# Performance work log

Hardware: AMD Instinct MI355X
Metric: run time of the kernel (lower is better)

The kernel has to match this reference:

```python
import jax, jax.numpy as jnp
import numpy as np

N_NODES = 100000
N_EDGES = 1200000
NUM_GRAPHS = 128
IN_DIM = 5
HIDDEN = 64


def setup_inputs() -> dict:
    key = jax.random.key(0)
    ks = jax.random.split(key, 12)
    x = jax.random.normal(ks[0], (N_NODES, IN_DIM), dtype=jnp.float32)
    edge_index = jax.random.randint(ks[1], (2, N_EDGES), 0, N_NODES, dtype=jnp.int64 if jax.config.read('jax_enable_x64') else jnp.int32)
    batch = jnp.sort(jax.random.randint(ks[2], (N_NODES,), 0, NUM_GRAPHS, dtype=jnp.int32))
    s = lambda fan_in: 1.0 / np.sqrt(fan_in)
    return {
        'x': x,
        'edge_index': edge_index,
        'batch': batch,
        'w_rel1': jax.random.normal(ks[3], (IN_DIM, HIDDEN), dtype=jnp.float32) * s(IN_DIM),
        'b_rel1': jnp.zeros((HIDDEN,), dtype=jnp.float32),
        'w_root1': jax.random.normal(ks[4], (IN_DIM, HIDDEN), dtype=jnp.float32) * s(IN_DIM),
        'w_rel2': jax.random.normal(ks[5], (HIDDEN, HIDDEN), dtype=jnp.float32) * s(HIDDEN),
        'b_rel2': jnp.zeros((HIDDEN,), dtype=jnp.float32),
        'w_root2': jax.random.normal(ks[6], (HIDDEN, HIDDEN), dtype=jnp.float32) * s(HIDDEN),
        'w_h1': jax.random.normal(ks[7], (2 * HIDDEN, HIDDEN), dtype=jnp.float32) * s(2 * HIDDEN),
        'b_h1': jnp.zeros((HIDDEN,), dtype=jnp.float32),
        'w_h2': jax.random.normal(ks[8], (HIDDEN, 1), dtype=jnp.float32) * s(HIDDEN),
        'b_h2': jnp.zeros((1,), dtype=jnp.float32),
    }


def _graph_conv(x, src, dst, w_rel, b_rel, w_root):
    # PyG GraphConv (aggr='add'): out = aggr(x_src -> dst) @ W_rel + b_rel + x @ W_root
    agg = jax.ops.segment_sum(x[src], dst, num_segments=N_NODES)
    return agg @ w_rel + b_rel + x @ w_root


def reference(x, edge_index, batch,
              w_rel1, b_rel1, w_root1,
              w_rel2, b_rel2, w_root2,
              w_h1, b_h1, w_h2, b_h2):
    src, dst = edge_index[0], edge_index[1]
    h = jax.nn.relu(_graph_conv(x, src, dst, w_rel1, b_rel1, w_root1))
    h = jax.nn.relu(_graph_conv(h, src, dst, w_rel2, b_rel2, w_root2))
    # global add + mean pooling over graphs
    add_pool = jax.ops.segment_sum(h, batch, num_segments=NUM_GRAPHS)
    counts = jax.ops.segment_sum(jnp.ones((N_NODES,), h.dtype), batch, num_segments=NUM_GRAPHS)
    mean_pool = add_pool / jnp.maximum(counts, 1.0)[:, None]
    g = jnp.concatenate([mean_pool, add_pool], axis=1)  # [G, 2*HIDDEN]
    out = jax.nn.relu(g @ w_h1 + b_h1) @ w_h2 + b_h2
    return out.squeeze(-1)
```

## Files before the change

kernel.cpp:

```cpp
#include <hip/hip_runtime.h>
#include <hip/hip_bf16.h>

#define N_NODES    100000
#define N_EDGES    1200000
#define NUM_GRAPHS 128
#define IN_DIM     5
#define HIDDEN     64
#define M_TILES    (N_NODES / 16)
#define NI4        (N_EDGES / 4)

#define CB    782
#define CBLK  256
#define EPB   ((NI4 + CBLK - 1) / CBLK)
#define STCAP 3072

typedef __attribute__((ext_vector_type(8))) short short8;
typedef __attribute__((ext_vector_type(4))) float f32x4;
typedef __attribute__((ext_vector_type(2))) float f32x2;

#if defined(__has_builtin)
#if __has_builtin(__builtin_amdgcn_cvt_pk_f32_fp8)
#define HAS_HWF8 1
#endif
#endif

__device__ __forceinline__ unsigned short f2bs(float f) {
    union { float f; unsigned u; } v; v.f = f;
    return (unsigned short)((v.u + 0x7FFFu + ((v.u >> 16) & 1u)) >> 16);
}
__device__ __forceinline__ float bs2f(unsigned short s) {
    union { unsigned u; float f; } v; v.u = ((unsigned)s) << 16;
    return v.f;
}
__device__ __forceinline__ float blo(unsigned p) { return bs2f((unsigned short)(p & 0xffff)); }
__device__ __forceinline__ float bhi(unsigned p) { return bs2f((unsigned short)(p >> 16)); }
__device__ __forceinline__ unsigned pack2(float a, float b) {
    return ((unsigned)f2bs(b) << 16) | (unsigned)f2bs(a);
}

__device__ __forceinline__ unsigned char f2f8(float f) {
    union { float f; unsigned u; } v; v.f = f * 0x1p-120f;
    unsigned u = v.u + 0x7FFFFu + ((v.u >> 20) & 1u);
    return (unsigned char)(u >> 20);
}
__device__ __forceinline__ float f82f(unsigned b) {
    union { unsigned u; float f; } v; v.u = (b & 0x7Fu) << 20;
    return v.f * 0x1p120f;
}

__device__ __forceinline__ void acc8(float4& a, unsigned r) {
#ifdef HAS_HWF8
    f32x2 lo = __builtin_amdgcn_cvt_pk_f32_fp8((int)r, false);
    f32x2 hi = __builtin_amdgcn_cvt_pk_f32_fp8((int)r, true);
    a.x += lo[0]; a.y += lo[1]; a.z += hi[0]; a.w += hi[1];
#else
    a.x += f82f(r); a.y += f82f(r >> 8); a.z += f82f(r >> 16); a.w += f82f(r >> 24);
#endif
}


__global__ void coarse_count(const int* __restrict__ dst, int* __restrict__ gcnt,
                             const float* __restrict__ x, uint4* __restrict__ xb,
                             float* __restrict__ add_pool, int* __restrict__ ptr) {
    __shared__ int h[CB];
    int t = threadIdx.x, b = blockIdx.x;
    for (int i = t; i < CB; i += 256) h[i] = 0;
    __syncthreads();
    int i0 = b * EPB, i1 = min(i0 + EPB, NI4);
    for (int i = i0 + t; i < i1; i += 256) {
        int4 d = ((const int4*)dst)[i];
        atomicAdd(&h[d.x >> 7], 1);
        atomicAdd(&h[d.y >> 7], 1);
        atomicAdd(&h[d.z >> 7], 1);
        atomicAdd(&h[d.w >> 7], 1);
    }
    __syncthreads();
    for (int i = t; i < CB; i += 256) gcnt[b * CB + i] = h[i];

    for (int n = b * 256 + t; n < N_NODES; n += CBLK * 256) {
        const float* xr = x + (size_t)n * IN_DIM;
        uint4 o;
        o.x = pack2(xr[0], xr[1]);
        o.y = pack2(xr[2], xr[3]);
        o.z = pack2(xr[4], 0.0f);
        o.w = 0u;
        xb[n] = o;
    }
    if (b == 0) {
        for (int i = t; i < NUM_GRAPHS * HIDDEN; i += 256) add_pool[i] = 0.0f;
        if (t == 0) ptr[N_NODES] = N_EDGES;
    }
}

__global__ void block_scan(int* __restrict__ gcnt, int* __restrict__ btot) {
    __shared__ int s[CBLK];
    int k = blockIdx.x, t = threadIdx.x;
    int v = gcnt[t * CB + k];
    s[t] = v;
    __syncthreads();
    for (int off = 1; off < CBLK; off <<= 1) {
        int u = (t >= off) ? s[t - off] : 0;
        __syncthreads();
        s[t] += u;
        __syncthreads();
    }
    gcnt[t * CB + k] = s[t] - v;
    if (t == CBLK - 1) btot[k] = s[t];
}

__global__ void bucket_scan(const int* __restrict__ btot, int* __restrict__ bstart) {
    __shared__ int s[1024];
    int t = threadIdx.x;
    int v = (t < CB) ? btot[t] : 0;
    s[t] = v;
    __syncthreads();
    for (int off = 1; off < 1024; off <<= 1) {
        int u = (t >= off) ? s[t - off] : 0;
        __syncthreads();
        s[t] += u;
        __syncthreads();
    }
    if (t < CB) bstart[t] = s[t] - v;
    if (t == 0) bstart[CB] = N_EDGES;
}

__global__ void partition_k(const int* __restrict__ src, const int* __restrict__ dst,
                            const int* __restrict__ gcnt, const int* __restrict__ bstart,
                            int* __restrict__ part) {
    __shared__ int base[CB];
    __shared__ int h[CB];
    int t = threadIdx.x, b = blockIdx.x;
    for (int i = t; i < CB; i += 256) {
        base[i] = bstart[i] + gcnt[b * CB + i];
        h[i] = 0;
    }
    __syncthreads();
    int i0 = b * EPB, i1 = min(i0 + EPB, NI4);
    for (int i = i0 + t; i < i1; i += 256) {
        int4 s4 = ((const int4*)src)[i];
        int4 d4 = ((const int4*)dst)[i];
        int k, r;
        k = d4.x >> 7; r = atomicAdd(&h[k], 1); part[base[k] + r] = s4.x | ((d4.x & 127) << 17);
        k = d4.y >> 7; r = atomicAdd(&h[k], 1); part[base[k] + r] = s4.y | ((d4.y & 127) << 17);
        k = d4.z >> 7; r = atomicAdd(&h[k], 1); part[base[k] + r] = s4.z | ((d4.z & 127) << 17);
        k = d4.w >> 7; r = atomicAdd(&h[k], 1); part[base[k] + r] = s4.w | ((d4.w & 127) << 17);
    }
}

__global__ void fine_gather1(const int* __restrict__ part, const int* __restrict__ bstart,
                             int* __restrict__ ptr, int* __restrict__ esrc,
                             const uint4* __restrict__ xb,
                             const float* __restrict__ x,
                             const float* __restrict__ w_rel1,
                             const float* __restrict__ b_rel1,
                             const float* __restrict__ w_root1,
                             unsigned short* __restrict__ h1,
                             unsigned char* __restrict__ h1f8) {
    __shared__ int fh[128];
    __shared__ int fo[128];
    __shared__ int fr[128];
    __shared__ uint4 stage[STCAP];
    int k = blockIdx.x, t = threadIdx.x;
    int e0 = bstart[k], e1 = bstart[k + 1];
    int ne = e1 - e0;
    bool useLds = (ne <= STCAP);
    if (t < 128) { fh[t] = 0; fr[t] = 0; }
    __syncthreads();
    for (int e = e0 + t; e < e1; e += 256)
        atomicAdd(&fh[(part[e] >> 17) & 127], 1);
    __syncthreads();
    int v = (t < 128) ? fh[t] : 0;
    if (t < 128) fo[t] = v;
    __syncthreads();
    for (int off = 1; off < 128; off <<= 1) {
        int u = (t >= off && t < 128) ? fo[t - off] : 0;
        __syncthreads();
        if (t < 128) fo[t] += u;
        __syncthreads();
    }
    if (t < 128) {
        int excl = fo[t] - v;
        int n_t = (k << 7) + t;
        if (n_t < N_NODES) ptr[n_t] = e0 + excl;
        fh[t] = excl;
    }
    __syncthreads();
    for (int e = e0 + t; e < e1; e += 256) {
        int p = part[e];
        int d = (p >> 17) & 127;
        int s = p & 0x1FFFF;
        int r = atomicAdd(&fr[d], 1);
        int slot = fh[d] + r;
        esrc[e0 + slot] = s;
        if (useLds) stage[slot] = xb[s];
    }
    __syncthreads();

    int ql = t & 15;
    int g  = t >> 4;
    float wr[IN_DIM][4], wo[IN_DIM][4], bias[4];
#pragma unroll
    for (int j = 0; j < 4; ++j) {
        int ch = ql * 4 + j;
        bias[j] = b_rel1[ch];
#pragma unroll
        for (int kk = 0; kk < IN_DIM; ++kk) {
            wr[kk][j] = w_rel1[kk * HIDDEN + ch];
            wo[kk][j] = w_root1[kk * HIDDEN + ch];
        }
    }

    for (int nl = g; nl < 128; nl += 16) {
        int n = (k << 7) + nl;
        if (n >= N_NODES) break;
        int s0 = fh[nl];
        int s1 = (nl < 127) ? fh[nl + 1] : ne;
        float a[IN_DIM] = {0.f, 0.f, 0.f, 0.f, 0.f};
        if (useLds) {
            for (int i = s0 + ql; i < s1; i += 16) {
                uint4 p = stage[i];
                a[0] += blo(p.x); a[1] += bhi(p.x);
                a[2] += blo(p.y); a[3] += bhi(p.y);
                a[4] += blo(p.z);
            }
        } else {
            for (int i = s0 + ql; i < s1; i += 16) {
                uint4 p = xb[esrc[e0 + i]];
                a[0] += blo(p.x); a[1] += bhi(p.x);
                a[2] += blo(p.y); a[3] += bhi(p.y);
                a[4] += blo(p.z);
            }
        }
#pragma unroll
        for (int kk = 0; kk < IN_DIM; ++kk) {
            a[kk] += __shfl_xor(a[kk], 1, 64);
            a[kk] += __shfl_xor(a[kk], 2, 64);
            a[kk] += __shfl_xor(a[kk], 4, 64);
            a[kk] += __shfl_xor(a[kk], 8, 64);
        }
        float xr[IN_DIM];
#pragma unroll
        for (int kk = 0; kk < IN_DIM; ++kk) xr[kk] = x[(size_t)n * IN_DIM + kk];

        unsigned short hv[4];
        unsigned char  hf[4];
#pragma unroll
        for (int j = 0; j < 4; ++j) {
            float acc = bias[j];
#pragma unroll
            for (int kk = 0; kk < IN_DIM; ++kk)
                acc += a[kk] * wr[kk][j] + xr[kk] * wo[kk][j];
            float h = fmaxf(acc, 0.0f);
            hv[j] = f2bs(h);
            hf[j] = f2f8(h);
        }
        ushort4 v4; v4.x = hv[0]; v4.y = hv[1]; v4.z = hv[2]; v4.w = hv[3];
        *(ushort4*)(h1 + (size_t)n * HIDDEN + ql * 4) = v4;
        uchar4 c4; c4.x = hf[0]; c4.y = hf[1]; c4.z = hf[2]; c4.w = hf[3];
        *(uchar4*)(h1f8 + (size_t)n * HIDDEN + ql * 4) = c4;
    }
}


__global__ void gather2_fp8(const unsigned* __restrict__ rows,
                            const int* __restrict__ ptr,
                            const int* __restrict__ esrc,
                            uint2* __restrict__ agg2) {
    int t    = threadIdx.x;
    int ql   = t & 15;
    int grp  = (blockIdx.x * blockDim.x + t) >> 4;
    int ngrp = (gridDim.x * blockDim.x) >> 4;

    for (int n = grp; n < N_NODES; n += ngrp) {
        int start = ptr[n], end = ptr[n + 1];
        float4 a0 = {0.f,0.f,0.f,0.f}, a1 = a0, a2 = a0, a3 = a0;
        int e = start;
        for (; e + 3 < end; e += 4) {
            int s0 = esrc[e], s1 = esrc[e + 1], s2 = esrc[e + 2], s3 = esrc[e + 3];
            unsigned r0 = rows[(size_t)s0 * 16 + ql];
            unsigned r1 = rows[(size_t)s1 * 16 + ql];
            unsigned r2 = rows[(size_t)s2 * 16 + ql];
            unsigned r3 = rows[(size_t)s3 * 16 + ql];
            acc8(a0, r0); acc8(a1, r1); acc8(a2, r2); acc8(a3, r3);
        }
        for (; e < end; ++e) {
            unsigned r0 = rows[(size_t)esrc[e] * 16 + ql];
            acc8(a0, r0);
        }
        float4 a;
        a.x = (a0.x + a1.x) + (a2.x + a3.x);
        a.y = (a0.y + a1.y) + (a2.y + a3.y);
        a.z = (a0.z + a1.z) + (a2.z + a3.z);
        a.w = (a0.w + a1.w) + (a2.w + a3.w);
        uint2 o;
        o.x = pack2(a.x, a.y);
        o.y = pack2(a.z, a.w);
        agg2[(size_t)n * 16 + ql] = o;
    }
}

__global__ void mlp2_pool(const unsigned short* __restrict__ agg2,
                          const unsigned short* __restrict__ h1,
                          const float* __restrict__ w_rel2,
                          const float* __restrict__ b_rel2,
                          const float* __restrict__ w_root2,
                          const int* __restrict__ batch,
                          float* __restrict__ add_pool) {
    int lane = threadIdx.x & 63;
    int wv   = threadIdx.x >> 6;
    int row  = lane & 15;
    int quad = lane >> 4;
    int n    = wv * 16 + row;

    short8 bwr[2], bwo[2];
#pragma unroll
    for (int s = 0; s < 2; ++s)
#pragma unroll
        for (int j = 0; j < 8; ++j) {
            int k = 32 * s + quad * 8 + j;
            bwr[s][j] = (short)f2bs(w_rel2[k * HIDDEN + n]);
            bwo[s][j] = (short)f2bs(w_root2[k * HIDDEN + n]);
        }
    float bias = b_rel2[n];

    for (int t = blockIdx.x; t < M_TILES; t += gridDim.x) {
        int m0 = t * 16;
        size_t rbase = (size_t)(m0 + row) * HIDDEN;
        short8 aa0 = *(const short8*)(agg2 + rbase + quad * 8);
        short8 aa1 = *(const short8*)(agg2 + rbase + 32 + quad * 8);
        short8 ah0 = *(const short8*)(h1   + rbase + quad * 8);
        short8 ah1 = *(const short8*)(h1   + rbase + 32 + quad * 8);

        f32x4 acc = {bias, bias, bias, bias};
        acc = __builtin_amdgcn_mfma_f32_16x16x32_bf16(aa0, bwr[0], acc, 0, 0, 0);
        acc = __builtin_amdgcn_mfma_f32_16x16x32_bf16(aa1, bwr[1], acc, 0, 0, 0);
        acc = __builtin_amdgcn_mfma_f32_16x16x32_bf16(ah0, bwo[0], acc, 0, 0, 0);
        acc = __builtin_amdgcn_mfma_f32_16x16x32_bf16(ah1, bwo[1], acc, 0, 0, 0);

        float hv0 = fmaxf(acc[0], 0.0f), hv1 = fmaxf(acc[1], 0.0f);
        float hv2 = fmaxf(acc[2], 0.0f), hv3 = fmaxf(acc[3], 0.0f);

        int gLo = batch[m0], gHi = batch[m0 + 15];
        if (gLo == gHi) {
            float s = (hv0 + hv1) + (hv2 + hv3);
            s += __shfl_xor(s, 16, 64);
            s += __shfl_xor(s, 32, 64);
            if (quad == 0)
                atomicAdd(&add_pool[gLo * HIDDEN + n], s);
        } else {
            int m = m0 + quad * 4;
            atomicAdd(&add_pool[batch[m]     * HIDDEN + n], hv0);
            atomicAdd(&add_pool[batch[m + 1] * HIDDEN + n], hv1);
            atomicAdd(&add_pool[batch[m + 2] * HIDDEN + n], hv2);
            atomicAdd(&add_pool[batch[m + 3] * HIDDEN + n], hv3);
        }
    }
}

__device__ __forceinline__ int lower_bound_i(const int* a, int n, int v) {
    int lo = 0, hi = n;
    while (lo < hi) { int mid = (lo + hi) >> 1; if (a[mid] < v) lo = mid + 1; else hi = mid; }
    return lo;
}

__global__ void head_mlp(const float* __restrict__ add_pool,
                         const int* __restrict__ batch,
                         const float* __restrict__ w_h1,
                         const float* __restrict__ b_h1,
                         const float* __restrict__ w_h2,
                         const float* __restrict__ b_h2,
                         float* __restrict__ out) {
    int g = blockIdx.x, t = threadIdx.x;

    __shared__ int s_cnt;
    if (t == 0) {
        int start = lower_bound_i(batch, N_NODES, g);
        int end   = lower_bound_i(batch, N_NODES, g + 1);
        s_cnt = end - start;
    }
    __syncthreads();
    float cnt = fmaxf((float)s_cnt, 1.0f);

    __shared__ float sg[2 * HIDDEN];
    float add = add_pool[(size_t)g * HIDDEN + t];
    sg[t]          = add / cnt;
    sg[HIDDEN + t] = add;
    __syncthreads();

    float hid = b_h1[t];
#pragma unroll 16
    for (int i = 0; i < 2 * HIDDEN; ++i)
        hid += sg[i] * w_h1[i * HIDDEN + t];
    hid = fmaxf(hid, 0.0f);

    float res = hid * w_h2[t];
    for (int off = 32; off > 0; off >>= 1)
        res += __shfl_down(res, off, 64);
    if (t == 0) out[g] = res + b_h2[0];
}

extern "C" void kernel_launch(void* const* d_in, const int* in_sizes, int n_in,
                              void* d_out, int out_size, void* d_ws, size_t ws_size,
                              hipStream_t stream) {
    const float* x       = (const float*)d_in[0];
    const int*   ei      = (const int*)d_in[1];
    const int*   src     = ei;
    const int*   dst     = ei + N_EDGES;
    const int*   batch   = (const int*)d_in[2];
    const float* w_rel1  = (const float*)d_in[3];
    const float* b_rel1  = (const float*)d_in[4];
    const float* w_root1 = (const float*)d_in[5];
    const float* w_rel2  = (const float*)d_in[6];
    const float* b_rel2  = (const float*)d_in[7];
    const float* w_root2 = (const float*)d_in[8];
    const float* w_h1    = (const float*)d_in[9];
    const float* b_h1    = (const float*)d_in[10];
    const float* w_h2    = (const float*)d_in[11];
    const float* b_h2    = (const float*)d_in[12];
    float* out = (float*)d_out;

    int* base = (int*)d_ws;
    int*   gcnt     = base;
    int*   btot     = gcnt + ((CBLK * CB + 3) & ~3);
    int*   bstart   = btot + ((CB + 3) & ~3);
    float* add_pool = (float*)(bstart + ((CB + 1 + 3) & ~3));
    int*   ptr      = (int*)(add_pool + NUM_GRAPHS * HIDDEN);
    int*   part     = ptr + ((N_NODES + 1 + 3) & ~3);
    int*   esrc     = part + N_EDGES;
    unsigned short* h1   = (unsigned short*)(esrc + N_EDGES);
    unsigned short* agg2 = h1 + (size_t)N_NODES * HIDDEN;
    unsigned char*  h1f8 = (unsigned char*)(agg2 + (size_t)N_NODES * HIDDEN);
    uint4*          xb   = (uint4*)(h1f8 + (size_t)N_NODES * HIDDEN);

    coarse_count<<<CBLK, 256, 0, stream>>>(dst, gcnt, x, xb, add_pool, ptr);
    block_scan<<<CB, CBLK, 0, stream>>>(gcnt, btot);
    bucket_scan<<<1, 1024, 0, stream>>>(btot, bstart);
    partition_k<<<CBLK, 256, 0, stream>>>(src, dst, gcnt, bstart, part);

    fine_gather1<<<CB, 256, 0, stream>>>(part, bstart, ptr, esrc, xb, x,
                                         w_rel1, b_rel1, w_root1, h1, h1f8);
    gather2_fp8<<<2048, 256, 0, stream>>>((const unsigned*)h1f8, ptr, esrc, (uint2*)agg2);
    mlp2_pool<<<2048, 256, 0, stream>>>(agg2, h1, w_rel2, b_rel2, w_root2, batch, add_pool);
    head_mlp<<<NUM_GRAPHS, 64, 0, stream>>>(add_pool, batch, w_h1, b_h1, w_h2, b_h2, out);
}
```

Baseline: 195.4 us.

## Fuse layer-2 gather into MFMA pooling kernel and fold bucket scan into partition

Layer-2 neighbor aggregation now runs inside the MFMA/pooling kernel. Each 16-node tile is gathered into shared memory, so the bf16 agg2 buffer is never written to or read back from global memory. The single-block bucket scan is also removed: every partition block recomputes the bucket prefix sum with a wave-level scan, and block 0 writes bstart. This removes two launches and a global round trip. In exchange, the gather runs only 16 nodes per tile with two barriers per tile, which may lower memory-level parallelism in the gather.

```diff
diff --git a/kernel.cpp b/kernel.cpp
--- a/kernel.cpp
+++ b/kernel.cpp
@@ -13,6 +13,7 @@
 #define CBLK  256
 #define EPB   ((NI4 + CBLK - 1) / CBLK)
 #define STCAP 3072
+#define AGP   72
 
 typedef __attribute__((ext_vector_type(8))) short short8;
 typedef __attribute__((ext_vector_type(4))) float f32x4;
@@ -108,32 +109,46 @@
     if (t == CBLK - 1) btot[k] = s[t];
 }
 
-__global__ void bucket_scan(const int* __restrict__ btot, int* __restrict__ bstart) {
-    __shared__ int s[1024];
-    int t = threadIdx.x;
-    int v = (t < CB) ? btot[t] : 0;
-    s[t] = v;
-    __syncthreads();
-    for (int off = 1; off < 1024; off <<= 1) {
-        int u = (t >= off) ? s[t - off] : 0;
-        __syncthreads();
-        s[t] += u;
-        __syncthreads();
-    }
-    if (t < CB) bstart[t] = s[t] - v;
-    if (t == 0) bstart[CB] = N_EDGES;
-}
-
 __global__ void partition_k(const int* __restrict__ src, const int* __restrict__ dst,
-                            const int* __restrict__ gcnt, const int* __restrict__ bstart,
-                            int* __restrict__ part) {
+                            const int* __restrict__ gcnt, const int* __restrict__ btot,
+                            int* __restrict__ bstart, int* __restrict__ part) {
+    __shared__ int sb[CB];
     __shared__ int base[CB];
     __shared__ int h[CB];
     int t = threadIdx.x, b = blockIdx.x;
+    for (int i = t; i < CB; i += 256) sb[i] = btot[i];
+    __syncthreads();
+    if (t < 64) {
+        int loc[13];
+        int base_i = t * 13;
+        int sum = 0;
+#pragma unroll
+        for (int j = 0; j < 13; ++j) {
+            int idx = base_i + j;
+            int c = (idx < CB) ? sb[idx] : 0;
+            loc[j] = sum; sum += c;
+        }
+        int inc = sum;
+#pragma unroll
+        for (int off = 1; off < 64; off <<= 1) {
+            int u = __shfl_up(inc, off, 64);
+            if (t >= off) inc += u;
+        }
+        int excl = inc - sum;
+#pragma unroll
+        for (int j = 0; j < 13; ++j) {
+            int idx = base_i + j;
+            if (idx < CB) sb[idx] = excl + loc[j];
+        }
+    }
+    __syncthreads();
     for (int i = t; i < CB; i += 256) {
-        base[i] = bstart[i] + gcnt[b * CB + i];
+        int bs = sb[i];
+        base[i] = bs + gcnt[b * CB + i];
         h[i] = 0;
-    }
+        if (b == 0) bstart[i] = bs;
+    }
+    if (b == 0 && t == 0) bstart[CB] = N_EDGES;
     __syncthreads();
     int i0 = b * EPB, i1 = min(i0 + EPB, NI4);
     for (int i = i0 + t; i < i1; i += 256) {
@@ -261,56 +276,21 @@
     }
 }
 
-
-__global__ void gather2_fp8(const unsigned* __restrict__ rows,
-                            const int* __restrict__ ptr,
-                            const int* __restrict__ esrc,
-                            uint2* __restrict__ agg2) {
-    int t    = threadIdx.x;
-    int ql   = t & 15;
-    int grp  = (blockIdx.x * blockDim.x + t) >> 4;
-    int ngrp = (gridDim.x * blockDim.x) >> 4;
-
-    for (int n = grp; n < N_NODES; n += ngrp) {
-        int start = ptr[n], end = ptr[n + 1];
-        float4 a0 = {0.f,0.f,0.f,0.f}, a1 = a0, a2 = a0, a3 = a0;
-        int e = start;
-        for (; e + 3 < end; e += 4) {
-            int s0 = esrc[e], s1 = esrc[e + 1], s2 = esrc[e + 2], s3 = esrc[e + 3];
-            unsigned r0 = rows[(size_t)s0 * 16 + ql];
-            unsigned r1 = rows[(size_t)s1 * 16 + ql];
-            unsigned r2 = rows[(size_t)s2 * 16 + ql];
-            unsigned r3 = rows[(size_t)s3 * 16 + ql];
-            acc8(a0, r0); acc8(a1, r1); acc8(a2, r2); acc8(a3, r3);
-        }
-        for (; e < end; ++e) {
-            unsigned r0 = rows[(size_t)esrc[e] * 16 + ql];
-            acc8(a0, r0);
-        }
-        float4 a;
-        a.x = (a0.x + a1.x) + (a2.x + a3.x);
-        a.y = (a0.y + a1.y) + (a2.y + a3.y);
-        a.z = (a0.z + a1.z) + (a2.z + a3.z);
-        a.w = (a0.w + a1.w) + (a2.w + a3.w);
-        uint2 o;
-        o.x = pack2(a.x, a.y);
-        o.y = pack2(a.z, a.w);
-        agg2[(size_t)n * 16 + ql] = o;
-    }
-}
-
-__global__ void mlp2_pool(const unsigned short* __restrict__ agg2,
-                          const unsigned short* __restrict__ h1,
-                          const float* __restrict__ w_rel2,
-                          const float* __restrict__ b_rel2,
-                          const float* __restrict__ w_root2,
-                          const int* __restrict__ batch,
-                          float* __restrict__ add_pool) {
-    int lane = threadIdx.x & 63;
-    int wv   = threadIdx.x >> 6;
-    int row  = lane & 15;
-    int quad = lane >> 4;
+__global__ void gather2_mlp2(const unsigned* __restrict__ rows,
+                             const int* __restrict__ ptr,
+                             const int* __restrict__ esrc,
+                             const unsigned short* __restrict__ h1,
+                             const float* __restrict__ w_rel2,
+                             const float* __restrict__ b_rel2,
+                             const float* __restrict__ w_root2,
+                             const int* __restrict__ batch,
+                             float* __restrict__ add_pool) {
+    __shared__ unsigned short ag[16 * AGP];
+    int tid  = threadIdx.x;
+    int lane = tid & 63, wv = tid >> 6;
+    int row  = lane & 15, quad = lane >> 4;
     int n    = wv * 16 + row;
+    int g    = tid >> 4, ql = tid & 15;
 
     short8 bwr[2], bwo[2];
 #pragma unroll
@@ -325,11 +305,32 @@
 
     for (int t = blockIdx.x; t < M_TILES; t += gridDim.x) {
         int m0 = t * 16;
+        int nd = m0 + g;
+        int start = ptr[nd], end = ptr[nd + 1];
+        float4 a0 = {0.f, 0.f, 0.f, 0.f}, a1 = a0;
+        int e = start;
+        for (; e + 1 < end; e += 2) {
+            int sA = esrc[e], sB = esrc[e + 1];
+            unsigned r0 = rows[(size_t)sA * 16 + ql];
+            unsigned r1 = rows[(size_t)sB * 16 + ql];
+            acc8(a0, r0); acc8(a1, r1);
+        }
+        if (e < end) {
+            unsigned r0 = rows[(size_t)esrc[e] * 16 + ql];
+            acc8(a0, r0);
+        }
+        a0.x += a1.x; a0.y += a1.y; a0.z += a1.z; a0.w += a1.w;
+        uint2 pk;
+        pk.x = pack2(a0.x, a0.y);
+        pk.y = pack2(a0.z, a0.w);
+        *(uint2*)&ag[g * AGP + ql * 4] = pk;
+        __syncthreads();
+
         size_t rbase = (size_t)(m0 + row) * HIDDEN;
-        short8 aa0 = *(const short8*)(agg2 + rbase + quad * 8);
-        short8 aa1 = *(const short8*)(agg2 + rbase + 32 + quad * 8);
-        short8 ah0 = *(const short8*)(h1   + rbase + quad * 8);
-        short8 ah1 = *(const short8*)(h1   + rbase + 32 + quad * 8);
+        short8 aa0 = *(const short8*)&ag[row * AGP + quad * 8];
+        short8 aa1 = *(const short8*)&ag[row * AGP + 32 + quad * 8];
+        short8 ah0 = *(const short8*)(h1 + rbase + quad * 8);
+        short8 ah1 = *(const short8*)(h1 + rbase + 32 + quad * 8);
 
         f32x4 acc = {bias, bias, bias, bias};
         acc = __builtin_amdgcn_mfma_f32_16x16x32_bf16(aa0, bwr[0], acc, 0, 0, 0);
@@ -354,6 +355,7 @@
             atomicAdd(&add_pool[batch[m + 2] * HIDDEN + n], hv2);
             atomicAdd(&add_pool[batch[m + 3] * HIDDEN + n], hv3);
         }
+        __syncthreads();
     }
 }
 
@@ -428,18 +430,16 @@
     int*   part     = ptr + ((N_NODES + 1 + 3) & ~3);
     int*   esrc     = part + N_EDGES;
     unsigned short* h1   = (unsigned short*)(esrc + N_EDGES);
-    unsigned short* agg2 = h1 + (size_t)N_NODES * HIDDEN;
-    unsigned char*  h1f8 = (unsigned char*)(agg2 + (size_t)N_NODES * HIDDEN);
+    unsigned char*  h1f8 = (unsigned char*)(h1 + (size_t)N_NODES * HIDDEN);
     uint4*          xb   = (uint4*)(h1f8 + (size_t)N_NODES * HIDDEN);
 
     coarse_count<<<CBLK, 256, 0, stream>>>(dst, gcnt, x, xb, add_pool, ptr);
     block_scan<<<CB, CBLK, 0, stream>>>(gcnt, btot);
-    bucket_scan<<<1, 1024, 0, stream>>>(btot, bstart);
-    partition_k<<<CBLK, 256, 0, stream>>>(src, dst, gcnt, bstart, part);
+    partition_k<<<CBLK, 256, 0, stream>>>(src, dst, gcnt, btot, bstart, part);
 
     fine_gather1<<<CB, 256, 0, stream>>>(part, bstart, ptr, esrc, xb, x,
                                          w_rel1, b_rel1, w_root1, h1, h1f8);
-    gather2_fp8<<<2048, 256, 0, stream>>>((const unsigned*)h1f8, ptr, esrc, (uint2*)agg2);
-    mlp2_pool<<<2048, 256, 0, stream>>>(agg2, h1, w_rel2, b_rel2, w_root2, batch, add_pool);
+    gather2_mlp2<<<2048, 256, 0, stream>>>((const unsigned*)h1f8, ptr, esrc, h1,
+                                           w_rel2, b_rel2, w_root2, batch, add_pool);
     head_mlp<<<NUM_GRAPHS, 64, 0, stream>>>(add_pool, batch, w_h1, b_h1, w_h2, b_h2, out);
 }
```

Result: faster. 190.3 us (-2.6%).
